# Kernel optimization log

Measured on AMD Instinct MI355X. Metric: run time of the kernel, lower is better.

## Reference

```python
import jax, jax.numpy as jnp
import numpy as np

IDENTITY_WEIGHT = 0.5
EPS_NORM = 1e-6   # channel RMSNorm eps
EPS_COS = 1e-12   # cosine-sim norm eps (matches torch F.normalize default)


def setup_inputs() -> dict:
    key = jax.random.key(0)
    k1, k2 = jax.random.split(key)
    B, C, H, W = 32, 768, 32, 32
    X = jax.random.normal(k1, (B, C, H, W), dtype=jnp.float32)
    # 1x1 conv weight [out=3C, in=C] (kernel dims squeezed)
    W_in = jax.random.normal(k2, (3 * C, C), dtype=jnp.float32) * (C ** -0.5)
    return {"X": X, "W_in": W_in}


def _cos_sim(t):
    # normalize over the flattened spatial axis (last dim)
    return t / (jnp.linalg.norm(t, axis=-1, keepdims=True) + EPS_COS)


def reference(X, W_in):
    B, C, H, W = X.shape
    # norm: parameter-free RMS over channel dim
    Xn = X * jax.lax.rsqrt(jnp.mean(X * X, axis=1, keepdims=True) + EPS_NORM)
    # 1x1 conv (bias-free) == channel GEMM: [B,3C,H,W]
    qkv = jnp.einsum('oc,bchw->bohw', W_in, Xn)
    K = qkv[:, :C].reshape(B, 1, C, H * W)       # b h c (x y), h=1
    V = qkv[:, C:2 * C].reshape(B, 1, C, H * W)
    # cosine similarity per channel over spatial positions: [B,1,C,1]
    A = jnp.sum(_cos_sim(K) * _cos_sim(V), axis=-1, keepdims=True)
    # affine gate with identity weight (feature_map_attn = identity)
    A = (1.0 - IDENTITY_WEIGHT) * A + IDENTITY_WEIGHT
    A = A.reshape(B, C, 1, 1)  # 'b 1 c 1 -> b c 1 1'
    return A * X
```

## Files before the change

kernel.cpp:

```cpp
#include <hip/hip_runtime.h>
#include <cstdint>
#include <cstddef>


#define B_   32
#define C_   768
#define HW_  1024
#define CHW_ (C_ * HW_)
#define EPS_NORM 1e-6f
#define EPS_COS  1e-12f

using f32x4  = __attribute__((ext_vector_type(4))) float;
using bf16x8 = __attribute__((ext_vector_type(8))) short;

__device__ inline unsigned short f2bf(float f) {
    union { float f; unsigned u; } v; v.f = f;
    unsigned u = v.u;
    u += 0x7fffu + ((u >> 16) & 1u);
    return (unsigned short)(u >> 16);
}

__device__ __forceinline__ void load16_lds(const unsigned short* g, short* l) {
    __builtin_amdgcn_global_load_lds(
        (const __attribute__((address_space(1))) unsigned int*)g,
        (__attribute__((address_space(3))) unsigned int*)l,
        16, 0, 0);
}

__device__ __forceinline__ void stage_half(const unsigned short* g, short* l,
                                           size_t toff, int ldsoff, int rs) {
    load16_lds(g + toff,                     l + ldsoff);
    load16_lds(g + toff + (size_t)rs * 768,  l + ldsoff + 4096);
}

__global__ void wconv_kernel(const float* __restrict__ W, unsigned short* __restrict__ Wst) {
    const int orow = blockIdx.x;
    const int c4   = threadIdx.x;
    const int irow = (orow & 1) * 768 + (orow >> 1);
    const float4 v = reinterpret_cast<const float4*>(W + (size_t)irow * 768)[c4];
    ushort4 o;
    o.x = f2bf(v.x); o.y = f2bf(v.y); o.z = f2bf(v.z); o.w = f2bf(v.w);
    reinterpret_cast<ushort4*>(Wst + (size_t)orow * 768)[c4] = o;
}

__global__ void sumsq_kernel(const float* __restrict__ X, float* __restrict__ ssum) {
    const int b  = blockIdx.y;
    const int c0 = blockIdx.x * 32;
    const int t  = threadIdx.x;
    const float4* xp = reinterpret_cast<const float4*>(X + (size_t)b * CHW_ + (size_t)c0 * HW_) + t;
    float4 s = {0.f, 0.f, 0.f, 0.f};
    #pragma unroll 8
    for (int c = 0; c < 32; ++c) {
        float4 v = xp[c * 256];
        s.x += v.x * v.x; s.y += v.y * v.y; s.z += v.z * v.z; s.w += v.w * v.w;
    }
    float* dst = ssum + b * HW_ + t * 4;
    atomicAdd(dst + 0, s.x);
    atomicAdd(dst + 1, s.y);
    atomicAdd(dst + 2, s.z);
    atomicAdd(dst + 3, s.w);
}

__global__ __launch_bounds__(256) void xnt_kernel(const float* __restrict__ X,
                                                  const float* __restrict__ ssum,
                                                  unsigned short* __restrict__ Xnt) {
    const int b   = blockIdx.z;
    const int c0  = blockIdx.y * 64;
    const int hw0 = blockIdx.x * 64;
    const int tid = threadIdx.x;
    __shared__ short T[64][78];

    #pragma unroll
    for (int it = 0; it < 4; ++it) {
        int q  = it * 256 + tid;
        int r  = q >> 4;
        int c4 = (q & 15) * 4;
        const float4 x = *reinterpret_cast<const float4*>(
            X + (size_t)b * CHW_ + (size_t)(c0 + r) * HW_ + hw0 + c4);
        const float4 s = *reinterpret_cast<const float4*>(ssum + b * HW_ + hw0 + c4);
        ushort4 o;
        o.x = f2bf(x.x * rsqrtf(s.x * (1.f / 768.f) + EPS_NORM));
        o.y = f2bf(x.y * rsqrtf(s.y * (1.f / 768.f) + EPS_NORM));
        o.z = f2bf(x.z * rsqrtf(s.z * (1.f / 768.f) + EPS_NORM));
        o.w = f2bf(x.w * rsqrtf(s.w * (1.f / 768.f) + EPS_NORM));
        *reinterpret_cast<ushort4*>(&T[r][c4]) = o;
    }
    __syncthreads();
    #pragma unroll
    for (int it = 0; it < 2; ++it) {
        int q  = it * 256 + tid;
        int rp = q >> 3;
        int cc = (q & 7) * 8;
        __align__(16) unsigned short tmp[8];
        #pragma unroll
        for (int j = 0; j < 8; ++j) tmp[j] = (unsigned short)T[cc + j][rp];
        *reinterpret_cast<uint4*>(
            Xnt + (size_t)b * CHW_ + (size_t)(hw0 + rp) * C_ + c0 + cc) =
            *reinterpret_cast<const uint4*>(tmp);
    }
}

template<int P, bool VM>
__device__ __forceinline__ void phase(const short* Ar, const short* Br,
        const unsigned short* gs, short* ls, size_t toff, int ldsoff, int rs,
        int l15, int wgm64, int wnl64, int slot0, int slot1,
        bf16x8 (&bA)[2][2], bf16x8 (&bB)[4][2], f32x4 (&acc)[8][4]) {
    if constexpr (P == 0) {
        #pragma unroll
        for (int ni = 0; ni < 4; ++ni) {
            const int rB = wnl64 + (ni << 4) + l15;
            bB[ni][0] = *reinterpret_cast<const bf16x8*>(Br + (rB << 6) + slot0);
            bB[ni][1] = *reinterpret_cast<const bf16x8*>(Br + (rB << 6) + slot1);
        }
    }
    #pragma unroll
    for (int s = 0; s < 2; ++s) {
        const int rA = ((((P & 1) << 1) | s) << 4) + l15 + wgm64;
        bA[s][0] = *reinterpret_cast<const bf16x8*>(Ar + (rA << 6) + slot0);
        bA[s][1] = *reinterpret_cast<const bf16x8*>(Ar + (rA << 6) + slot1);
    }
    stage_half(gs, ls, toff, ldsoff, rs);
    if (VM) asm volatile("s_waitcnt vmcnt(6)" ::: "memory");
    __builtin_amdgcn_sched_barrier(0);
    __builtin_amdgcn_s_barrier();
    asm volatile("s_waitcnt lgkmcnt(0)" ::: "memory");
    __builtin_amdgcn_sched_barrier(0);
    __builtin_amdgcn_s_setprio(1);
    #pragma unroll
    for (int s = 0; s < 2; ++s)
        #pragma unroll
        for (int ni = 0; ni < 4; ++ni) {
            acc[(P << 1) | s][ni] = __builtin_amdgcn_mfma_f32_16x16x32_bf16(
                bA[s][0], bB[ni][0], acc[(P << 1) | s][ni], 0, 0, 0);
            acc[(P << 1) | s][ni] = __builtin_amdgcn_mfma_f32_16x16x32_bf16(
                bA[s][1], bB[ni][1], acc[(P << 1) | s][ni], 0, 0, 0);
        }
    __builtin_amdgcn_s_setprio(0);
    __builtin_amdgcn_sched_barrier(0);
    __builtin_amdgcn_s_barrier();
    __builtin_amdgcn_sched_barrier(0);
}

__global__ __launch_bounds__(512, 2) void gemm_kernel(
        const unsigned short* __restrict__ Wst,
        const unsigned short* __restrict__ Xnt,
        float* __restrict__ wsA) {
    const int n0   = blockIdx.x * 256;
    const int c0   = blockIdx.y * 256;
    const int b    = blockIdx.z;
    const int tid  = threadIdx.x;
    const int lane = tid & 63;
    const int wave = tid >> 6;
    const int l15  = lane & 15;
    const int quad = lane >> 4;
    const int wgm64 = (wave >> 2) << 6;
    const int wq    = wave & 3;
    const int wnl64 = (wq & 1) << 6;
    const int hB    = wq >> 1;

    const int lb7   = l15 & 7;
    const int slot0 = (quad ^ lb7) << 3;
    const int slot1 = ((quad + 4) ^ lb7) << 3;

    __shared__ __align__(16) short sA[2][2][128][64];
    __shared__ __align__(16) short sB[2][2][128][64];

    const int r0      = tid >> 3;
    const size_t toff = (size_t)r0 * 768 + (((tid & 7) ^ (r0 & 7)) << 3);
    const int ldsoff  = (r0 & ~7) << 6;

    const unsigned short* Ab = Wst + (size_t)c0 * 768;
    const unsigned short* Bb = Xnt + (size_t)b * CHW_ + (size_t)n0 * 768;

    f32x4 acc[8][4];
    const f32x4 zero = {0.f, 0.f, 0.f, 0.f};
    #pragma unroll
    for (int i = 0; i < 8; ++i)
        #pragma unroll
        for (int j = 0; j < 4; ++j) acc[i][j] = zero;

    bf16x8 bA[2][2], bB[4][2];

    stage_half(Ab,                &sA[0][0][0][0], toff, ldsoff, 128);
    stage_half(Ab + 64 * 768,     &sA[0][1][0][0], toff, ldsoff, 128);
    stage_half(Bb,                &sB[0][0][0][0], toff, ldsoff, 64);
    stage_half(Bb + 128 * 768,    &sB[0][1][0][0], toff, ldsoff, 64);
    stage_half(Bb + 64,           &sB[1][0][0][0], toff, ldsoff, 64);
    stage_half(Bb + 128 * 768 + 64, &sB[1][1][0][0], toff, ldsoff, 64);
    stage_half(Ab + 64,           &sA[1][0][0][0], toff, ldsoff, 128);
    asm volatile("s_waitcnt vmcnt(6)" ::: "memory");
    __builtin_amdgcn_s_barrier();
    __builtin_amdgcn_sched_barrier(0);

    for (int it = 0; it < 6; ++it) {
        const int kT1 = it * 128 + 64;
        int kT2 = it * 128 + 128; if (kT2 >= 768) kT2 -= 768;
        int kT3 = it * 128 + 192; if (kT3 >= 768) kT3 -= 768;

        phase<0, false>(&sA[0][0][0][0], &sB[0][hB][0][0],
                        Ab + 64 * 768 + kT1, &sA[1][1][0][0], toff, ldsoff, 128,
                        l15, wgm64, wnl64, slot0, slot1, bA, bB, acc);
        phase<1, false>(&sA[0][0][0][0], nullptr,
                        Bb + kT2,            &sB[0][0][0][0], toff, ldsoff, 64,
                        l15, wgm64, wnl64, slot0, slot1, bA, bB, acc);
        phase<2, false>(&sA[0][1][0][0], nullptr,
                        Bb + 128 * 768 + kT2, &sB[0][1][0][0], toff, ldsoff, 64,
                        l15, wgm64, wnl64, slot0, slot1, bA, bB, acc);
        phase<3, true >(&sA[0][1][0][0], nullptr,
                        Ab + kT2,            &sA[0][0][0][0], toff, ldsoff, 128,
                        l15, wgm64, wnl64, slot0, slot1, bA, bB, acc);
        phase<0, false>(&sA[1][0][0][0], &sB[1][hB][0][0],
                        Ab + 64 * 768 + kT2, &sA[0][1][0][0], toff, ldsoff, 128,
                        l15, wgm64, wnl64, slot0, slot1, bA, bB, acc);
        phase<1, false>(&sA[1][0][0][0], nullptr,
                        Bb + kT3,            &sB[1][0][0][0], toff, ldsoff, 64,
                        l15, wgm64, wnl64, slot0, slot1, bA, bB, acc);
        phase<2, false>(&sA[1][1][0][0], nullptr,
                        Bb + 128 * 768 + kT3, &sB[1][1][0][0], toff, ldsoff, 64,
                        l15, wgm64, wnl64, slot0, slot1, bA, bB, acc);
        phase<3, true >(&sA[1][1][0][0], nullptr,
                        Ab + kT3,            &sA[1][0][0][0], toff, ldsoff, 128,
                        l15, wgm64, wnl64, slot0, slot1, bA, bB, acc);
    }
    asm volatile("s_waitcnt vmcnt(0)" ::: "memory");

    #pragma unroll
    for (int mi = 0; mi < 8; ++mi) {
        float d0 = 0.f, e0 = 0.f, f0 = 0.f, d1 = 0.f, e1 = 0.f, f1 = 0.f;
        #pragma unroll
        for (int ni = 0; ni < 4; ++ni) {
            f32x4 a = acc[mi][ni];
            d0 += a[0] * a[1]; e0 += a[0] * a[0]; f0 += a[1] * a[1];
            d1 += a[2] * a[3]; e1 += a[2] * a[2]; f1 += a[3] * a[3];
        }
        #pragma unroll
        for (int off = 1; off < 16; off <<= 1) {
            d0 += __shfl_xor(d0, off); e0 += __shfl_xor(e0, off); f0 += __shfl_xor(f0, off);
            d1 += __shfl_xor(d1, off); e1 += __shfl_xor(e1, off); f1 += __shfl_xor(f1, off);
        }
        if (l15 == 0) {
            const int ch = (c0 >> 1) + wgm64 + (mi << 3) + (quad << 1);
            float* dst = wsA + ((size_t)b * C_ + ch) * 3;
            atomicAdd(dst + 0, d0); atomicAdd(dst + 1, e0); atomicAdd(dst + 2, f0);
            atomicAdd(dst + 3, d1); atomicAdd(dst + 4, e1); atomicAdd(dst + 5, f1);
        }
    }
}

__global__ void final_kernel(const float* __restrict__ X, const float* __restrict__ wsA,
                             float* __restrict__ out) {
    const int bc = blockIdx.x;
    const float* a = wsA + (size_t)bc * 3;
    const float pd = a[0], pk = a[1], pv = a[2];
    const float A = pd / ((sqrtf(pk) + EPS_COS) * (sqrtf(pv) + EPS_COS));
    const float g = 0.5f * A + 0.5f;
    const size_t i4 = (size_t)bc * 256 + threadIdx.x;
    float4 x = reinterpret_cast<const float4*>(X)[i4];
    float4 o;
    o.x = x.x * g; o.y = x.y * g; o.z = x.z * g; o.w = x.w * g;
    reinterpret_cast<float4*>(out)[i4] = o;
}

extern "C" void kernel_launch(void* const* d_in, const int* in_sizes, int n_in,
                              void* d_out, int out_size, void* d_ws, size_t ws_size,
                              hipStream_t stream) {
    const float* X = (const float*)d_in[0];
    const float* W = (const float*)d_in[1];
    float* out = (float*)d_out;

    char* ws = (char*)d_ws;
    float* wsA           = (float*)ws;
    float* ssum          = (float*)(ws + 294912);
    unsigned short* Wst  = (unsigned short*)(ws + 425984);
    unsigned short* Xnt  = (unsigned short*)(ws + 2785280);

    hipMemsetAsync(ws, 0, 425984, stream);

    wconv_kernel<<<dim3(1536),       192, 0, stream>>>(W, Wst);
    sumsq_kernel<<<dim3(24, 32),     256, 0, stream>>>(X, ssum);
    xnt_kernel  <<<dim3(16, 12, 32), 256, 0, stream>>>(X, ssum, Xnt);
    gemm_kernel <<<dim3(4, 6, 32),   512, 0, stream>>>(Wst, Xnt, wsA);
    final_kernel<<<dim3(24576),      256, 0, stream>>>(X, wsA, out);
}
```

Baseline: 325.1 us.

## Fuse sumsq and normalize kernels, remap GEMM blocks per XCD, batch final scaling

Merges the channel sum-of-squares pass and the normalize/transpose pass into one kernel. Each block computes the RMS scale for its 64 spatial positions in shared memory, then loops over all 12 channel chunks, which removes the ssum atomics and part of the memset. The GEMM grid is flattened and remapped so blocks sharing a batch/N-tile land on the same XCD for L2 reuse. The final kernel processes 8 channels per block. The fused norm kernel launches only 512 blocks and reads X twice inside one block, so it has less parallelism and may lose memory-level concurrency.

```diff
diff --git a/kernel.cpp b/kernel.cpp
--- a/kernel.cpp
+++ b/kernel.cpp
@@ -43,60 +43,71 @@
     reinterpret_cast<ushort4*>(Wst + (size_t)orow * 768)[c4] = o;
 }
 
-__global__ void sumsq_kernel(const float* __restrict__ X, float* __restrict__ ssum) {
-    const int b  = blockIdx.y;
-    const int c0 = blockIdx.x * 32;
-    const int t  = threadIdx.x;
-    const float4* xp = reinterpret_cast<const float4*>(X + (size_t)b * CHW_ + (size_t)c0 * HW_) + t;
-    float4 s = {0.f, 0.f, 0.f, 0.f};
-    #pragma unroll 8
-    for (int c = 0; c < 32; ++c) {
-        float4 v = xp[c * 256];
-        s.x += v.x * v.x; s.y += v.y * v.y; s.z += v.z * v.z; s.w += v.w * v.w;
-    }
-    float* dst = ssum + b * HW_ + t * 4;
-    atomicAdd(dst + 0, s.x);
-    atomicAdd(dst + 1, s.y);
-    atomicAdd(dst + 2, s.z);
-    atomicAdd(dst + 3, s.w);
-}
-
-__global__ __launch_bounds__(256) void xnt_kernel(const float* __restrict__ X,
-                                                  const float* __restrict__ ssum,
-                                                  unsigned short* __restrict__ Xnt) {
-    const int b   = blockIdx.z;
-    const int c0  = blockIdx.y * 64;
+__global__ __launch_bounds__(256) void norm_kernel(const float* __restrict__ X,
+                                                   unsigned short* __restrict__ Xnt) {
+    const int b   = blockIdx.y;
     const int hw0 = blockIdx.x * 64;
     const int tid = threadIdx.x;
-    __shared__ short T[64][78];
-
-    #pragma unroll
-    for (int it = 0; it < 4; ++it) {
-        int q  = it * 256 + tid;
-        int r  = q >> 4;
-        int c4 = (q & 15) * 4;
-        const float4 x = *reinterpret_cast<const float4*>(
-            X + (size_t)b * CHW_ + (size_t)(c0 + r) * HW_ + hw0 + c4);
-        const float4 s = *reinterpret_cast<const float4*>(ssum + b * HW_ + hw0 + c4);
-        ushort4 o;
-        o.x = f2bf(x.x * rsqrtf(s.x * (1.f / 768.f) + EPS_NORM));
-        o.y = f2bf(x.y * rsqrtf(s.y * (1.f / 768.f) + EPS_NORM));
-        o.z = f2bf(x.z * rsqrtf(s.z * (1.f / 768.f) + EPS_NORM));
-        o.w = f2bf(x.w * rsqrtf(s.w * (1.f / 768.f) + EPS_NORM));
-        *reinterpret_cast<ushort4*>(&T[r][c4]) = o;
-    }
+    __shared__ float4 P[256];
+    __shared__ short  T[64][78];
+
+    const int cg = tid >> 4;
+    const int q4 = tid & 15;
+    const float* xb = X + (size_t)b * CHW_ + hw0 + q4 * 4;
+    float4 s = {0.f, 0.f, 0.f, 0.f};
+    #pragma unroll 4
+    for (int c = cg; c < 768; c += 16) {
+        float4 v = *reinterpret_cast<const float4*>(xb + (size_t)c * HW_);
+        s.x += v.x * v.x; s.y += v.y * v.y; s.z += v.z * v.z; s.w += v.w * v.w;
+    }
+    P[tid] = s;
     __syncthreads();
-    #pragma unroll
-    for (int it = 0; it < 2; ++it) {
-        int q  = it * 256 + tid;
-        int rp = q >> 3;
-        int cc = (q & 7) * 8;
-        __align__(16) unsigned short tmp[8];
-        #pragma unroll
-        for (int j = 0; j < 8; ++j) tmp[j] = (unsigned short)T[cc + j][rp];
-        *reinterpret_cast<uint4*>(
-            Xnt + (size_t)b * CHW_ + (size_t)(hw0 + rp) * C_ + c0 + cc) =
-            *reinterpret_cast<const uint4*>(tmp);
+    if (tid < 16) {
+        float4 a = P[tid];
+        #pragma unroll
+        for (int g = 1; g < 16; ++g) {
+            float4 v = P[g * 16 + tid];
+            a.x += v.x; a.y += v.y; a.z += v.z; a.w += v.w;
+        }
+        float4 sc;
+        sc.x = rsqrtf(a.x * (1.f / 768.f) + EPS_NORM);
+        sc.y = rsqrtf(a.y * (1.f / 768.f) + EPS_NORM);
+        sc.z = rsqrtf(a.z * (1.f / 768.f) + EPS_NORM);
+        sc.w = rsqrtf(a.w * (1.f / 768.f) + EPS_NORM);
+        P[tid] = sc;
+    }
+    __syncthreads();
+
+    #pragma unroll 1
+    for (int ch = 0; ch < 12; ++ch) {
+        const int c0 = ch * 64;
+        #pragma unroll
+        for (int it = 0; it < 4; ++it) {
+            int q  = it * 256 + tid;
+            int r  = q >> 4;
+            int c4 = (q & 15) * 4;
+            const float4 x = *reinterpret_cast<const float4*>(
+                X + (size_t)b * CHW_ + (size_t)(c0 + r) * HW_ + hw0 + c4);
+            const float4 sc = P[q & 15];
+            ushort4 o;
+            o.x = f2bf(x.x * sc.x); o.y = f2bf(x.y * sc.y);
+            o.z = f2bf(x.z * sc.z); o.w = f2bf(x.w * sc.w);
+            *reinterpret_cast<ushort4*>(&T[r][c4]) = o;
+        }
+        __syncthreads();
+        #pragma unroll
+        for (int it = 0; it < 2; ++it) {
+            int q  = it * 256 + tid;
+            int rp = q >> 3;
+            int cc = (q & 7) * 8;
+            __align__(16) unsigned short tmp[8];
+            #pragma unroll
+            for (int j = 0; j < 8; ++j) tmp[j] = (unsigned short)T[cc + j][rp];
+            *reinterpret_cast<uint4*>(
+                Xnt + (size_t)b * CHW_ + (size_t)(hw0 + rp) * C_ + c0 + cc) =
+                *reinterpret_cast<const uint4*>(tmp);
+        }
+        __syncthreads();
     }
 }
 
@@ -145,9 +156,15 @@
         const unsigned short* __restrict__ Wst,
         const unsigned short* __restrict__ Xnt,
         float* __restrict__ wsA) {
-    const int n0   = blockIdx.x * 256;
-    const int c0   = blockIdx.y * 256;
-    const int b    = blockIdx.z;
+    const int h     = blockIdx.x;
+    const int xcd   = h & 7;
+    const int w     = h >> 3;
+    const int slice = ((w / 6) << 3) + xcd;
+    const int memb  = w % 6;
+    const int n0    = (slice & 3) * 256;
+    const int c0    = memb * 256;
+    const int b     = slice >> 2;
+
     const int tid  = threadIdx.x;
     const int lane = tid & 63;
     const int wave = tid >> 6;
@@ -247,18 +264,23 @@
     }
 }
 
-__global__ void final_kernel(const float* __restrict__ X, const float* __restrict__ wsA,
-                             float* __restrict__ out) {
-    const int bc = blockIdx.x;
-    const float* a = wsA + (size_t)bc * 3;
-    const float pd = a[0], pk = a[1], pv = a[2];
-    const float A = pd / ((sqrtf(pk) + EPS_COS) * (sqrtf(pv) + EPS_COS));
-    const float g = 0.5f * A + 0.5f;
-    const size_t i4 = (size_t)bc * 256 + threadIdx.x;
-    float4 x = reinterpret_cast<const float4*>(X)[i4];
-    float4 o;
-    o.x = x.x * g; o.y = x.y * g; o.z = x.z * g; o.w = x.w * g;
-    reinterpret_cast<float4*>(out)[i4] = o;
+__global__ __launch_bounds__(256) void final_kernel(const float* __restrict__ X,
+                                                    const float* __restrict__ wsA,
+                                                    float* __restrict__ out) {
+    const int bc0 = blockIdx.x * 8;
+    const int tid = threadIdx.x;
+    #pragma unroll
+    for (int j = 0; j < 8; ++j) {
+        const int bc = bc0 + j;
+        const float* a = wsA + (size_t)bc * 3;
+        const float pd = a[0], pk = a[1], pv = a[2];
+        const float g = 0.5f * (pd / ((sqrtf(pk) + EPS_COS) * (sqrtf(pv) + EPS_COS))) + 0.5f;
+        const size_t i4 = (size_t)bc * 256 + tid;
+        float4 x = reinterpret_cast<const float4*>(X)[i4];
+        float4 o;
+        o.x = x.x * g; o.y = x.y * g; o.z = x.z * g; o.w = x.w * g;
+        reinterpret_cast<float4*>(out)[i4] = o;
+    }
 }
 
 extern "C" void kernel_launch(void* const* d_in, const int* in_sizes, int n_in,
@@ -270,15 +292,13 @@
 
     char* ws = (char*)d_ws;
     float* wsA           = (float*)ws;
-    float* ssum          = (float*)(ws + 294912);
     unsigned short* Wst  = (unsigned short*)(ws + 425984);
     unsigned short* Xnt  = (unsigned short*)(ws + 2785280);
 
-    hipMemsetAsync(ws, 0, 425984, stream);
-
-    wconv_kernel<<<dim3(1536),       192, 0, stream>>>(W, Wst);
-    sumsq_kernel<<<dim3(24, 32),     256, 0, stream>>>(X, ssum);
-    xnt_kernel  <<<dim3(16, 12, 32), 256, 0, stream>>>(X, ssum, Xnt);
-    gemm_kernel <<<dim3(4, 6, 32),   512, 0, stream>>>(Wst, Xnt, wsA);
-    final_kernel<<<dim3(24576),      256, 0, stream>>>(X, wsA, out);
-}
+    hipMemsetAsync(ws, 0, 294912, stream);
+
+    wconv_kernel<<<dim3(1536),   192, 0, stream>>>(W, Wst);
+    norm_kernel <<<dim3(16, 32), 256, 0, stream>>>(X, Xnt);
+    gemm_kernel <<<dim3(768),    512, 0, stream>>>(Wst, Xnt, wsA);
+    final_kernel<<<dim3(3072),   256, 0, stream>>>(X, wsA, out);
+}
```

Measured after the change: 323.6 us. No clear change (-0.5%).
